# Performance work log

Hardware: AMD Instinct MI355X
Metric: run time of the kernel (lower is better)

The kernel has to match this reference:

```python
import jax, jax.numpy as jnp
import numpy as np
from jax import lax


def setup_inputs() -> dict:
    key = jax.random.key(0)
    k1, k2, k3, k4 = jax.random.split(key, 4)
    H = 2048
    L = 3
    hidden_states = jax.random.normal(k1, (2, 4096, H), dtype=jnp.float32)
    Win = jax.random.normal(k2, (3 * H, H), dtype=jnp.float32) * (H ** -0.5)
    conv_w = jax.random.normal(k3, (H, 1, L), dtype=jnp.float32) * (L ** -0.5)
    Wout = jax.random.normal(k4, (H, H), dtype=jnp.float32) * (H ** -0.5)
    return {"hidden_states": hidden_states, "Win": Win, "conv_w": conv_w, "Wout": Wout}


def reference(hidden_states, Win, conv_w, Wout):
    H = hidden_states.shape[-1]
    L = conv_w.shape[-1]
    BCx = jnp.einsum('bsh,oh->bso', hidden_states, Win)  # (b, s, 3H)
    B, C, x = jnp.split(BCx, 3, axis=-1)
    Bx = jnp.transpose(B * x, (0, 2, 1))  # (b, H, s)
    # depthwise causal conv: left-pad L-1 so output length == s (torch pads both
    # sides then slices [..., :seqlen]; left-only padding is equivalent)
    conv_out = lax.conv_general_dilated(
        Bx, conv_w, window_strides=(1,), padding=[(L - 1, 0)],
        feature_group_count=H, dimension_numbers=('NCH', 'OIH', 'NCH'))
    y = C * jnp.transpose(conv_out, (0, 2, 1))  # (b, s, H)
    return jnp.einsum('bsh,oh->bso', y, Wout)
```

## Files before the change

kernel.cpp:

```cpp
#include <hip/hip_runtime.h>
#include <hip/hip_bf16.h>

typedef unsigned short u16;
typedef __attribute__((ext_vector_type(8))) short bf16x8;
typedef __attribute__((ext_vector_type(4))) float f32x4;

static __device__ __forceinline__ u16 f2bf(float f) {
    unsigned u = __float_as_uint(f);
    unsigned r = (u + 0x7fffu + ((u >> 16) & 1u)) >> 16;
    return (u16)r;
}
static __device__ __forceinline__ float bf2f(u16 u) {
    return __uint_as_float(((unsigned)u) << 16);
}

static __device__ __forceinline__ void async_copy16(const void* gptr, void* lptr) {
    __builtin_amdgcn_global_load_lds(
        (const __attribute__((address_space(1))) void*)gptr,
        (__attribute__((address_space(3))) void*)lptr, 16, 0, 0);
}

__global__ __launch_bounds__(256)
void cvt_all(const float* __restrict__ a, const float* __restrict__ b,
             const float* __restrict__ c,
             u16* __restrict__ oa, u16* __restrict__ ob, u16* __restrict__ oc) {
#pragma unroll
    for (int it = 0; it < 8; it++) {
        long li = ((long)it << 20) + (long)blockIdx.x * 256 + threadIdx.x;
        const float* src; u16* dst; long u;
        if (li < 4194304)      { src = a; dst = oa; u = li; }
        else if (li < 7340032) { src = b; dst = ob; u = li - 4194304; }
        else                   { src = c; dst = oc; u = li - 7340032; }
        long i = u * 4;
        float4 f = *(const float4*)(src + i);
        u16 o[4] = { f2bf(f.x), f2bf(f.y), f2bf(f.z), f2bf(f.w) };
        *(uint2*)(dst + i) = *(const uint2*)o;
    }
}

template<bool BF16_OUT>
__global__ __launch_bounds__(512, 2)
void gemm_bt8(const u16* __restrict__ A, const u16* __restrict__ B,
              void* __restrict__ Cout, int M, int N, int K) {
    __shared__ __align__(16) u16 lds[65536];

    const int t    = threadIdx.x;
    const int lane = t & 63;
    const int wm   = (t >> 6) >> 2;
    const int wn   = (t >> 6) & 3;
    const int l15  = lane & 15;
    const int hi   = lane >> 4;
    const int l7   = lane & 7;

    const int id   = blockIdx.y * gridDim.x + blockIdx.x;
    const int cpx  = gridDim.x >> 3;
    const int bx   = (id & 7) * cpx + ((id >> 3) % cpx);
    const int by   = (id >> 3) / cpx;
    const long rowA = (long)by * 256;
    const long rowB = (long)bx * 256;

    const int pl0 = t >> 3;
    const int slotcol = ((t & 7) ^ (pl0 & 7)) * 8;
    const u16* Asrc[2][2]; const u16* Bsrc[2][2];
#pragma unroll
    for (int h = 0; h < 2; h++) {
        int gA0 = h * 64 + pl0;
        int gA1 = 128 + h * 64 + pl0;
        Asrc[h][0] = A + (rowA + gA0) * (long)K + slotcol;
        Asrc[h][1] = A + (rowA + gA1) * (long)K + slotcol;
        int nB0 = (pl0 >> 5) * 64 + h * 32 + (pl0 & 31);
        Bsrc[h][0] = B + (rowB + nB0) * (long)K + slotcol;
        Bsrc[h][1] = B + (rowB + nB0 + 128) * (long)K + slotcol;
    }
    const int t8 = t * 8;

    auto STAGE_A = [&](int bufo, int h, int kk) {
        u16* d = lds + bufo + h * 8192 + t8;
        async_copy16(Asrc[h][0] + kk, d);
        async_copy16(Asrc[h][1] + kk, d + 4096);
    };
    auto STAGE_B = [&](int bufo, int h, int kk) {
        u16* d = lds + bufo + 16384 + h * 8192 + t8;
        async_copy16(Bsrc[h][0] + kk, d);
        async_copy16(Bsrc[h][1] + kk, d + 4096);
    };

    const int aBase = wm * 4096 + l15 * 64;
    const int bBase = 16384 + wn * 2048 + l15 * 64;
    const int sOff0 = (hi ^ l7) * 8;
    const int sOff1 = ((4 + hi) ^ l7) * 8;

    bf16x8 af[4][2], ba[2][2], bb[2][2];
    f32x4 acc[8][4] = {};

    auto LOAD_A2 = [&](int bufo, int Mq, int mb) {
        const u16* p = lds + bufo + Mq * 8192 + aBase + mb * 1024;
        af[mb][0]     = *(const bf16x8*)(p + sOff0);
        af[mb][1]     = *(const bf16x8*)(p + sOff1);
        af[mb + 1][0] = *(const bf16x8*)(p + 1024 + sOff0);
        af[mb + 1][1] = *(const bf16x8*)(p + 1024 + sOff1);
    };
    auto LOAD_B = [&](bf16x8 (&bg)[2][2], int bufo, int Nq) {
        const u16* p = lds + bufo + Nq * 8192 + bBase;
        bg[0][0] = *(const bf16x8*)(p + sOff0);
        bg[0][1] = *(const bf16x8*)(p + sOff1);
        bg[1][0] = *(const bf16x8*)(p + 1024 + sOff0);
        bg[1][1] = *(const bf16x8*)(p + 1024 + sOff1);
    };
    auto MFMA_H = [&](int Mq, int Nq, int mb, bf16x8 (&bg)[2][2]) {
        __builtin_amdgcn_s_setprio(1);
#pragma unroll
        for (int ks = 0; ks < 2; ks++)
#pragma unroll
            for (int m = mb; m < mb + 2; m++)
#pragma unroll
                for (int n = 0; n < 2; n++)
                    acc[Mq * 4 + m][Nq * 2 + n] =
                        __builtin_amdgcn_mfma_f32_16x16x32_bf16(
                            af[m][ks], bg[n][ks], acc[Mq * 4 + m][Nq * 2 + n],
                            0, 0, 0);
        __builtin_amdgcn_s_setprio(0);
    };

#define BAR()   __builtin_amdgcn_s_barrier()
#define SB()    __builtin_amdgcn_sched_barrier(0)
#define LGKM(n) do { asm volatile("s_waitcnt lgkmcnt(" #n ")" ::: "memory"); \
                     __builtin_amdgcn_sched_barrier(0); } while (0)
#define VM(n)   asm volatile("s_waitcnt vmcnt(" #n ")" ::: "memory")

#define TILE(BC, BN, KK)                                                     \
                                                              \
    LOAD_B(ba, BC, 0); LOAD_A2(BC, 0, 0); SB(); LOAD_A2(BC, 0, 2);           \
    STAGE_A(BN, 0, KK); VM(2);                                               \
    LGKM(4); MFMA_H(0, 0, 0, ba); LGKM(0); MFMA_H(0, 0, 2, ba); BAR();       \
                                                              \
    LOAD_B(bb, BC, 1);                                                       \
    STAGE_B(BN, 0, KK);                                                      \
    LGKM(0); MFMA_H(0, 1, 0, bb); MFMA_H(0, 1, 2, bb); BAR();                \
                                                              \
    LOAD_A2(BC, 1, 0); SB(); LOAD_A2(BC, 1, 2);                              \
    STAGE_A(BN, 1, KK);                                                      \
    LGKM(4); MFMA_H(1, 1, 0, bb); LGKM(0); MFMA_H(1, 1, 2, bb); BAR();       \
                                                              \
    STAGE_B(BN, 1, KK); VM(4);                                               \
    MFMA_H(1, 0, 0, ba); MFMA_H(1, 0, 2, ba); BAR();

    STAGE_A(0, 0, 0);  STAGE_B(0, 0, 0);
    STAGE_A(0, 1, 0);  STAGE_B(0, 1, 0);
    asm volatile("s_waitcnt vmcnt(0)" ::: "memory");
    BAR();

    const int NT = K >> 6;
#pragma unroll 1
    for (int i = 0; i < NT; i += 2) {
        int k1 = (i + 1) << 6;
        int k2 = (i + 2 < NT) ? (i + 2) << 6 : 0;
        TILE(0, 32768, k1);
        TILE(32768, 0, k2);
    }
    asm volatile("s_waitcnt vmcnt(0) lgkmcnt(0)" ::: "memory");

#undef TILE
#undef VM
#undef LGKM
#undef SB
#undef BAR

    const long crowBase = rowA + wm * 128 + hi * 4;
    const long ccolBase = rowB + wn * 64 + l15;
#pragma unroll
    for (int mi = 0; mi < 8; mi++) {
#pragma unroll
        for (int nj = 0; nj < 4; nj++) {
            long base = (crowBase + mi * 16) * N + ccolBase + nj * 16;
#pragma unroll
            for (int r = 0; r < 4; r++) {
                float v = acc[mi][nj][r];
                long idx = base + (long)r * N;
                if (BF16_OUT) ((u16*)Cout)[idx] = f2bf(v);
                else          ((float*)Cout)[idx] = v;
            }
        }
    }
}

union U16x8 { uint4 v; u16 u[8]; };

__global__ __launch_bounds__(256)
void conv_fuse(const u16* __restrict__ BCx, const float* __restrict__ cw,
               u16* __restrict__ y) {
    const int r0 = blockIdx.x * 4;
    const int h0 = threadIdx.x * 8;
    const int batch = r0 >> 12;

    U16x8 Bv[6], Xv[6], Cv[4];
#pragma unroll
    for (int ii = 0; ii < 6; ii++) {
        int g = r0 - 2 + ii;
        if (g >= 0 && (g >> 12) == batch) {
            const u16* rp = BCx + (long)g * 6144;
            Bv[ii].v = *(const uint4*)(rp + h0);
            Xv[ii].v = *(const uint4*)(rp + 4096 + h0);
        } else {
            Bv[ii].v = make_uint4(0, 0, 0, 0);
            Xv[ii].v = make_uint4(0, 0, 0, 0);
        }
    }
#pragma unroll
    for (int jj = 0; jj < 4; jj++)
        Cv[jj].v = *(const uint4*)(BCx + (long)(r0 + jj) * 6144 + 2048 + h0);

    float bx[6][8];
#pragma unroll
    for (int ii = 0; ii < 6; ii++)
#pragma unroll
        for (int i = 0; i < 8; i++)
            bx[ii][i] = bf2f(Bv[ii].u[i]) * bf2f(Xv[ii].u[i]);

    float w0[8], w1[8], w2[8];
#pragma unroll
    for (int i = 0; i < 8; i++) {
        int h = h0 + i;
        w0[i] = cw[h * 3];
        w1[i] = cw[h * 3 + 1];
        w2[i] = cw[h * 3 + 2];
    }

#pragma unroll
    for (int jj = 0; jj < 4; jj++) {
        U16x8 o;
#pragma unroll
        for (int i = 0; i < 8; i++) {
            float v = w2[i] * bx[jj + 2][i] + w1[i] * bx[jj + 1][i]
                    + w0[i] * bx[jj][i];
            o.u[i] = f2bf(v * bf2f(Cv[jj].u[i]));
        }
        *(uint4*)(y + (long)(r0 + jj) * 2048 + h0) = o.v;
    }
}

extern "C" void kernel_launch(void* const* d_in, const int* in_sizes, int n_in,
                              void* d_out, int out_size, void* d_ws, size_t ws_size,
                              hipStream_t stream) {
    const float* hs   = (const float*)d_in[0];
    const float* Win  = (const float*)d_in[1];
    const float* cw   = (const float*)d_in[2];
    const float* Wout = (const float*)d_in[3];
    float* out = (float*)d_out;

    char* ws = (char*)d_ws;
    u16* hsb   = (u16*)(ws);
    u16* Winb  = (u16*)(ws +  33554432);
    u16* Woutb = (u16*)(ws +  58720256);
    u16* bcx   = (u16*)(ws +  67108864);
    u16* yb    = (u16*)(ws + 167772160);

    cvt_all<<<4096, 256, 0, stream>>>(hs, Win, Wout, hsb, Winb, Woutb);

    gemm_bt8<true ><<<dim3(24, 32), 512, 0, stream>>>(hsb, Winb, bcx, 8192, 6144, 2048);

    conv_fuse<<<2048, 256, 0, stream>>>(bcx, cw, yb);

    gemm_bt8<false><<<dim3(8, 32), 512, 0, stream>>>(yb, Woutb, out, 8192, 2048, 2048);
}
```

Baseline: 442.1 us.

## Fuse B*x product into input GEMM epilogue by interleaving B and x weight rows

The input projection GEMM now gives the first 16 column blocks a tile that loads 128 rows of the B weights and the matching 128 rows of the x weights. It multiplies the two accumulators in the epilogue and writes only B*x as bf16. The remaining blocks write C separately. This removes the bf16 write and re-read of a full x tensor and the separate B/x reads in the conv kernel. The conv kernel now handles 8 rows per block to reduce halo re-reads, at the cost of more register pressure from the extra row buffers.

New measurement: 413.2 us. -6.5%, faster.

```diff
diff --git a/kernel.cpp b/kernel.cpp
--- a/kernel.cpp
+++ b/kernel.cpp
@@ -38,10 +38,11 @@
     }
 }
 
-template<bool BF16_OUT>
+template<bool FUSED>
 __global__ __launch_bounds__(512, 2)
 void gemm_bt8(const u16* __restrict__ A, const u16* __restrict__ B,
-              void* __restrict__ Cout, int M, int N, int K) {
+              u16* __restrict__ oBx, u16* __restrict__ oC,
+              float* __restrict__ oF, int M, int N, int K) {
     __shared__ __align__(16) u16 lds[65536];
 
     const int t    = threadIdx.x;
@@ -57,7 +58,6 @@
     const int bx   = (id & 7) * cpx + ((id >> 3) % cpx);
     const int by   = (id >> 3) / cpx;
     const long rowA = (long)by * 256;
-    const long rowB = (long)bx * 256;
 
     const int pl0 = t >> 3;
     const int slotcol = ((t & 7) ^ (pl0 & 7)) * 8;
@@ -68,9 +68,22 @@
         int gA1 = 128 + h * 64 + pl0;
         Asrc[h][0] = A + (rowA + gA0) * (long)K + slotcol;
         Asrc[h][1] = A + (rowA + gA1) * (long)K + slotcol;
-        int nB0 = (pl0 >> 5) * 64 + h * 32 + (pl0 & 31);
-        Bsrc[h][0] = B + (rowB + nB0) * (long)K + slotcol;
-        Bsrc[h][1] = B + (rowB + nB0 + 128) * (long)K + slotcol;
+    }
+    if (FUSED && bx < 16) {
+        const long rB = (long)bx * 128 + pl0;
+        Bsrc[0][0] = B + rB * (long)K + slotcol;
+        Bsrc[0][1] = Bsrc[0][0] + 64 * (long)K;
+        Bsrc[1][0] = B + (4096 + rB) * (long)K + slotcol;
+        Bsrc[1][1] = Bsrc[1][0] + 64 * (long)K;
+    } else {
+        const long rowB = FUSED ? (2048 + (long)(bx - 16) * 256)
+                                : (long)bx * 256;
+#pragma unroll
+        for (int h = 0; h < 2; h++) {
+            int nB0 = (pl0 >> 5) * 64 + h * 32 + (pl0 & 31);
+            Bsrc[h][0] = B + (rowB + nB0) * (long)K + slotcol;
+            Bsrc[h][1] = Bsrc[h][0] + 128 * (long)K;
+        }
     }
     const int t8 = t * 8;
 
@@ -154,7 +167,7 @@
 #pragma unroll 1
     for (int i = 0; i < NT; i += 2) {
         int k1 = (i + 1) << 6;
-        int k2 = (i + 2 < NT) ? (i + 2) << 6 : 0;
+        int k2 = (i + 2 < NT) ? (i + 2) << 6 : k1;
         TILE(0, 32768, k1);
         TILE(32768, 0, k2);
     }
@@ -166,56 +179,71 @@
 #undef SB
 #undef BAR
 
-    const long crowBase = rowA + wm * 128 + hi * 4;
-    const long ccolBase = rowB + wn * 64 + l15;
-#pragma unroll
-    for (int mi = 0; mi < 8; mi++) {
-#pragma unroll
-        for (int nj = 0; nj < 4; nj++) {
-            long base = (crowBase + mi * 16) * N + ccolBase + nj * 16;
-#pragma unroll
-            for (int r = 0; r < 4; r++) {
-                float v = acc[mi][nj][r];
-                long idx = base + (long)r * N;
-                if (BF16_OUT) ((u16*)Cout)[idx] = f2bf(v);
-                else          ((float*)Cout)[idx] = v;
+    const long rBase = rowA + wm * 128 + hi * 4;
+    if (FUSED && bx < 16) {
+        const long hBase = (long)bx * 128 + wn * 32 + l15;
+#pragma unroll
+        for (int mi = 0; mi < 8; mi++) {
+#pragma unroll
+            for (int n = 0; n < 2; n++) {
+                long col = hBase + n * 16;
+#pragma unroll
+                for (int r = 0; r < 4; r++) {
+                    long row = rBase + mi * 16 + r;
+                    float v = acc[mi][n][r] * acc[mi][n + 2][r];
+                    oBx[row * 2048 + col] = f2bf(v);
+                }
             }
         }
+    } else if (FUSED) {
+        const long colBase = (long)(bx - 16) * 256 + wn * 64 + l15;
+#pragma unroll
+        for (int mi = 0; mi < 8; mi++)
+#pragma unroll
+            for (int nj = 0; nj < 4; nj++)
+#pragma unroll
+                for (int r = 0; r < 4; r++) {
+                    long row = rBase + mi * 16 + r;
+                    oC[row * 2048 + colBase + nj * 16] = f2bf(acc[mi][nj][r]);
+                }
+    } else {
+        const long colBase = (long)bx * 256 + wn * 64 + l15;
+#pragma unroll
+        for (int mi = 0; mi < 8; mi++)
+#pragma unroll
+            for (int nj = 0; nj < 4; nj++)
+#pragma unroll
+                for (int r = 0; r < 4; r++) {
+                    long row = rBase + mi * 16 + r;
+                    oF[row * (long)N + colBase + nj * 16] = acc[mi][nj][r];
+                }
     }
 }
 
 union U16x8 { uint4 v; u16 u[8]; };
 
 __global__ __launch_bounds__(256)
-void conv_fuse(const u16* __restrict__ BCx, const float* __restrict__ cw,
-               u16* __restrict__ y) {
-    const int r0 = blockIdx.x * 4;
+void conv_fuse(const u16* __restrict__ Bx, const u16* __restrict__ Cc,
+               const float* __restrict__ cw, u16* __restrict__ y) {
+    const int r0 = blockIdx.x * 8;
     const int h0 = threadIdx.x * 8;
     const int batch = r0 >> 12;
 
-    U16x8 Bv[6], Xv[6], Cv[4];
-#pragma unroll
-    for (int ii = 0; ii < 6; ii++) {
+    U16x8 P[10];
+#pragma unroll
+    for (int ii = 0; ii < 10; ii++) {
         int g = r0 - 2 + ii;
-        if (g >= 0 && (g >> 12) == batch) {
-            const u16* rp = BCx + (long)g * 6144;
-            Bv[ii].v = *(const uint4*)(rp + h0);
-            Xv[ii].v = *(const uint4*)(rp + 4096 + h0);
-        } else {
-            Bv[ii].v = make_uint4(0, 0, 0, 0);
-            Xv[ii].v = make_uint4(0, 0, 0, 0);
-        }
-    }
-#pragma unroll
-    for (int jj = 0; jj < 4; jj++)
-        Cv[jj].v = *(const uint4*)(BCx + (long)(r0 + jj) * 6144 + 2048 + h0);
-
-    float bx[6][8];
-#pragma unroll
-    for (int ii = 0; ii < 6; ii++)
+        if (g >= 0 && (g >> 12) == batch)
+            P[ii].v = *(const uint4*)(Bx + (long)g * 2048 + h0);
+        else
+            P[ii].v = make_uint4(0, 0, 0, 0);
+    }
+    float bx[10][8];
+#pragma unroll
+    for (int ii = 0; ii < 10; ii++)
 #pragma unroll
         for (int i = 0; i < 8; i++)
-            bx[ii][i] = bf2f(Bv[ii].u[i]) * bf2f(Xv[ii].u[i]);
+            bx[ii][i] = bf2f(P[ii].u[i]);
 
     float w0[8], w1[8], w2[8];
 #pragma unroll
@@ -227,13 +255,14 @@
     }
 
 #pragma unroll
-    for (int jj = 0; jj < 4; jj++) {
-        U16x8 o;
+    for (int jj = 0; jj < 8; jj++) {
+        U16x8 Cv, o;
+        Cv.v = *(const uint4*)(Cc + (long)(r0 + jj) * 2048 + h0);
 #pragma unroll
         for (int i = 0; i < 8; i++) {
             float v = w2[i] * bx[jj + 2][i] + w1[i] * bx[jj + 1][i]
                     + w0[i] * bx[jj][i];
-            o.u[i] = f2bf(v * bf2f(Cv[jj].u[i]));
+            o.u[i] = f2bf(v * bf2f(Cv.u[i]));
         }
         *(uint4*)(y + (long)(r0 + jj) * 2048 + h0) = o.v;
     }
@@ -252,14 +281,17 @@
     u16* hsb   = (u16*)(ws);
     u16* Winb  = (u16*)(ws +  33554432);
     u16* Woutb = (u16*)(ws +  58720256);
-    u16* bcx   = (u16*)(ws +  67108864);
-    u16* yb    = (u16*)(ws + 167772160);
+    u16* bxb   = (u16*)(ws +  67108864);
+    u16* cb    = (u16*)(ws + 100663296);
+    u16* yb    = (u16*)(ws + 134217728);
 
     cvt_all<<<4096, 256, 0, stream>>>(hs, Win, Wout, hsb, Winb, Woutb);
 
-    gemm_bt8<true ><<<dim3(24, 32), 512, 0, stream>>>(hsb, Winb, bcx, 8192, 6144, 2048);
-
-    conv_fuse<<<2048, 256, 0, stream>>>(bcx, cw, yb);
-
-    gemm_bt8<false><<<dim3(8, 32), 512, 0, stream>>>(yb, Woutb, out, 8192, 2048, 2048);
-}
+    gemm_bt8<true ><<<dim3(24, 32), 512, 0, stream>>>(
+        hsb, Winb, bxb, cb, nullptr, 8192, 2048, 2048);
+
+    conv_fuse<<<1024, 256, 0, stream>>>(bxb, cb, cw, yb);
+
+    gemm_bt8<false><<<dim3(8, 32), 512, 0, stream>>>(
+        yb, Woutb, nullptr, nullptr, out, 8192, 2048, 2048);
+}
```
